# Kernel tuning notes

Measured on AMD Instinct MI355X. Metric: run time of the kernel, lower is better.

The kernel has to match this reference:

```python
import jax, jax.numpy as jnp
import numpy as np

N_NODES = 10000
N_EDGES = 100000
IN_CH = 64
EDGE_DIM = 16
HID = 128
HEADS = 4
LAYERS = 4
NUM_GRAPHS = 256


def setup_inputs() -> dict:
    key = jax.random.key(0)
    ks = jax.random.split(key, 16)
    s = 0.1
    HC = HEADS * HID
    L = LAYERS
    return {
        "x": jax.random.normal(ks[0], (N_NODES, IN_CH), jnp.float32),
        "edge_index": jax.random.randint(ks[1], (2, N_EDGES), 0, N_NODES, dtype=jnp.int32),
        "edge_attr": jax.random.normal(ks[2], (N_EDGES, EDGE_DIM), jnp.float32),
        "batch": jnp.sort(jax.random.randint(ks[3], (N_NODES,), 0, NUM_GRAPHS, dtype=jnp.int32)),
        "Win": jax.random.normal(ks[4], (IN_CH, HID), jnp.float32) * s,
        "b_in": jnp.zeros((HID,), jnp.float32),
        "Wl": jax.random.normal(ks[5], (L, HID, HC), jnp.float32) * s,
        "bl": jnp.zeros((L, HC), jnp.float32),
        "Wr": jax.random.normal(ks[6], (L, HID, HC), jnp.float32) * s,
        "br": jnp.zeros((L, HC), jnp.float32),
        "We": jax.random.normal(ks[7], (L, EDGE_DIM, HC), jnp.float32) * s,
        "att": jax.random.normal(ks[8], (L, HEADS, HID), jnp.float32) * s,
        "b_gat": jnp.zeros((L, HID), jnp.float32),
        "gamma": jnp.ones((L, HID), jnp.float32),
        "beta": jnp.zeros((L, HID), jnp.float32),
        "Wres": jax.random.normal(ks[9], (L - 1, HID, HID), jnp.float32) * s,
        "bres": jnp.zeros((L - 1, HID), jnp.float32),
        "W1": jax.random.normal(ks[10], (HID, HID), jnp.float32) * s,
        "b1": jnp.zeros((HID,), jnp.float32),
        "W2": jax.random.normal(ks[11], (HID, HID // 2), jnp.float32) * s,
        "b2": jnp.zeros((HID // 2,), jnp.float32),
        "W3": jax.random.normal(ks[12], (HID // 2, 1), jnp.float32) * s,
        "b3": jnp.zeros((1,), jnp.float32),
    }


def _layer_norm(x, g, b):
    mu = x.mean(-1, keepdims=True)
    var = ((x - mu) ** 2).mean(-1, keepdims=True)
    return g * (x - mu) / jnp.sqrt(var + 1e-5) + b


def _gatv2(h, src, dst, edge_attr, Wl, bl, Wr, br, We, att, bias):
    # GATv2Conv, concat=False, share_weights=False, negative_slope=0.2, eval mode
    N = h.shape[0]
    H, C = att.shape
    xl = (h @ Wl + bl).reshape(N, H, C)   # source-side features (lin_l)
    xr = (h @ Wr + br).reshape(N, H, C)   # target-side features (lin_r)
    e = (edge_attr @ We).reshape(-1, H, C)
    m = xl[src] + xr[dst] + e             # [E, H, C]
    m = jnp.where(m > 0, m, 0.2 * m)      # leaky_relu
    logits = jnp.einsum('ehc,hc->eh', m, att)
    lmax = jax.lax.stop_gradient(jax.ops.segment_max(logits, dst, num_segments=N))
    p = jnp.exp(logits - lmax[dst])
    denom = jax.ops.segment_sum(p, dst, num_segments=N)
    alpha = p / (denom[dst] + 1e-16)      # segment softmax over in-edges of each target
    out = jax.ops.segment_sum(alpha[:, :, None] * xl[src], dst, num_segments=N)
    return out.mean(axis=1) + bias        # concat=False -> head mean, plus bias


def reference(x, edge_index, edge_attr, batch, Win, b_in, Wl, bl, Wr, br, We, att,
              b_gat, gamma, beta, Wres, bres, W1, b1, W2, b2, W3, b3):
    src, dst = edge_index[0], edge_index[1]
    h = jax.nn.elu(x @ Win + b_in)
    for i in range(LAYERS):
        h_res = h
        h = _gatv2(h, src, dst, edge_attr, Wl[i], bl[i], Wr[i], br[i], We[i], att[i], b_gat[i])
        h = jax.nn.elu(_layer_norm(h, gamma[i], beta[i]))
        if i > 0:
            h = h + (h_res @ Wres[i - 1] + bres[i - 1])
    sums = jax.ops.segment_sum(h, batch, num_segments=NUM_GRAPHS)
    counts = jax.ops.segment_sum(jnp.ones((h.shape[0], 1), h.dtype), batch, num_segments=NUM_GRAPHS)
    hg = sums / jnp.maximum(counts, 1.0)  # global_mean_pool
    z = jax.nn.relu(hg @ W1 + b1)
    z = jax.nn.relu(z @ W2 + b2)
    return (z @ W3 + b3).reshape(-1)
```

## Files before the change

kernel.cpp:

```cpp
#include <hip/hip_runtime.h>

#define N_NODES 10000
#define N_EDGES 100000
#define IN_CH 64
#define EDGE_DIM 16
#define HID 128
#define HEADS 4
#define HC 512
#define LAYERS 4
#define NUM_GRAPHS 256
#define NCAT 1152
#define LDP 136
#define ECHUNK 32

typedef __bf16 bf16;
typedef __bf16 bf16x8 __attribute__((ext_vector_type(8)));
typedef __bf16 bf16x4 __attribute__((ext_vector_type(4)));
typedef float floatx4 __attribute__((ext_vector_type(4)));
typedef float f32x2 __attribute__((ext_vector_type(2)));

__device__ __forceinline__ float elu_f(float x) { return x > 0.f ? x : (__expf(x) - 1.f); }

__global__ __launch_bounds__(128) void k_prep_w(
    const float* __restrict__ Wl, const float* __restrict__ bl,
    const float* __restrict__ Wr, const float* __restrict__ br,
    const float* __restrict__ Wres, const float* __restrict__ bres,
    bf16* __restrict__ WT, float* __restrict__ bcat) {
    __shared__ float tile[16][129];
    int nt = blockIdx.x, i = blockIdx.y, z = blockIdx.z;
    int t = threadIdx.x;
    int n0 = nt * 128;
    const float* base = nullptr; const float* bsrc = nullptr; int ld = 0;
    if (nt < 4)       { base = Wl + (size_t)i * HID * HC + n0;            bsrc = bl + i * HC + n0;              ld = HC; }
    else if (nt < 8)  { base = Wr + (size_t)i * HID * HC + (n0 - 512);    bsrc = br + i * HC + (n0 - 512);      ld = HC; }
    else if (i > 0)   { base = Wres + (size_t)(i - 1) * HID * HID;        bsrc = bres + (size_t)(i - 1) * HID;  ld = HID; }
    if (base) {
#pragma unroll
        for (int r = 0; r < 16; r++) tile[r][t] = base[(size_t)(z * 16 + r) * ld + t];
    } else {
#pragma unroll
        for (int r = 0; r < 16; r++) tile[r][t] = 0.f;
    }
    __syncthreads();
    int n = n0 + t;
    if (z == 0) bcat[(size_t)i * NCAT + n] = base ? bsrc[t] : 0.f;
    bf16* dst = WT + ((size_t)i * NCAT + n) * HID + z * 16;
#pragma unroll
    for (int kc = 0; kc < 2; kc++) {
        bf16x8 v;
#pragma unroll
        for (int u = 0; u < 8; u++) v[u] = (bf16)tile[kc * 8 + u][t];
        *(bf16x8*)(dst + kc * 8) = v;
    }
}

__global__ __launch_bounds__(128) void k_init_h(const float* __restrict__ x,
                                                const float* __restrict__ Win,
                                                const float* __restrict__ b_in,
                                                bf16* __restrict__ h_bf) {
    __shared__ float xs[IN_CH];
    int n = blockIdx.x, t = threadIdx.x;
    if (t < IN_CH) xs[t] = x[(size_t)n * IN_CH + t];
    __syncthreads();
    float s = b_in[t];
#pragma unroll 8
    for (int k = 0; k < IN_CH; k++) s = fmaf(xs[k], Win[k * HID + t], s);
    h_bf[(size_t)n * HID + t] = (bf16)elu_f(s);
}

__global__ __launch_bounds__(256, 2) void k_gemm_mfma(
    const bf16* __restrict__ A, const bf16* __restrict__ WT,
    const float* __restrict__ bcat, bf16* __restrict__ C, int M) {
    __shared__ __align__(16) unsigned short As[128 * LDP];
    __shared__ __align__(16) unsigned short Bs[128 * LDP];
    int t = threadIdx.x;
    int r0 = blockIdx.x * 128, c0 = blockIdx.y * 128;
#pragma unroll
    for (int i = 0; i < 8; i++) {
        int idx = t + i * 256;
        int row = idx >> 4;
        int ch = idx & 15;
        int r = r0 + row; if (r >= M) r = M - 1;
        uint4 va = *(const uint4*)(A + (size_t)r * HID + ch * 8);
        *(uint4*)&As[row * LDP + ch * 8] = va;
        uint4 vb = *(const uint4*)(WT + (size_t)(c0 + row) * HID + ch * 8);
        *(uint4*)&Bs[row * LDP + ch * 8] = vb;
    }
    __syncthreads();

    int wave = t >> 6, lane = t & 63;
    int wm = wave & 1, wn = wave >> 1;
    int quad = lane >> 4, lm = lane & 15;
    floatx4 zero = {0.f, 0.f, 0.f, 0.f};
    floatx4 acc[4][4];
#pragma unroll
    for (int mi = 0; mi < 4; mi++)
#pragma unroll
        for (int ni = 0; ni < 4; ni++) acc[mi][ni] = zero;

    const unsigned short* Ab = &As[(wm * 64 + lm) * LDP + quad * 8];
    const unsigned short* Bb = &Bs[(wn * 64 + lm) * LDP + quad * 8];
#pragma unroll
    for (int ks = 0; ks < 4; ks++) {
        bf16x8 af[4], bfr[4];
#pragma unroll
        for (int mi = 0; mi < 4; mi++) af[mi] = *(const bf16x8*)(Ab + mi * 16 * LDP + ks * 32);
#pragma unroll
        for (int ni = 0; ni < 4; ni++) bfr[ni] = *(const bf16x8*)(Bb + ni * 16 * LDP + ks * 32);
#pragma unroll
        for (int mi = 0; mi < 4; mi++)
#pragma unroll
            for (int ni = 0; ni < 4; ni++)
                acc[mi][ni] = __builtin_amdgcn_mfma_f32_16x16x32_bf16(bfr[ni], af[mi], acc[mi][ni], 0, 0, 0);
    }

#pragma unroll
    for (int mi = 0; mi < 4; mi++) {
        int row = r0 + wm * 64 + mi * 16 + lm;
        if (row < M) {
            bf16* crow = C + (size_t)row * NCAT;
#pragma unroll
            for (int ni = 0; ni < 4; ni++) {
                int cb = c0 + wn * 64 + ni * 16 + quad * 4;
                float4 b4 = *(const float4*)(bcat + cb);
                floatx4 v = acc[mi][ni];
                bf16x4 o = {(bf16)(v[0] + b4.x), (bf16)(v[1] + b4.y),
                            (bf16)(v[2] + b4.z), (bf16)(v[3] + b4.w)};
                *(bf16x4*)(crow + cb) = o;
            }
        }
    }
}

__global__ void k_degree(const int* __restrict__ ei, const int* __restrict__ batch,
                         int* __restrict__ deg, int* __restrict__ cnt) {
    int e = blockIdx.x * blockDim.x + threadIdx.x;
    if (e < N_EDGES) atomicAdd(&deg[ei[N_EDGES + e]], 1);
    if (e < N_NODES) atomicAdd(&cnt[batch[e]], 1);
}

__global__ __launch_bounds__(1024) void k_scan(const int* __restrict__ deg,
                                               int* __restrict__ row_start,
                                               int* __restrict__ cursor) {
    __shared__ int wsum[16];
    __shared__ int carry_s;
    int t = threadIdx.x;
    int wave = t >> 6, lane = t & 63;
    if (t == 0) { carry_s = 0; row_start[0] = 0; }
    __syncthreads();
    for (int base = 0; base < N_NODES; base += 1024) {
        int i = base + t;
        int v = (i < N_NODES) ? deg[i] : 0;
        int incl = v;
#pragma unroll
        for (int off = 1; off < 64; off <<= 1) {
            int u = __shfl_up(incl, off, 64);
            if (lane >= off) incl += u;
        }
        if (lane == 63) wsum[wave] = incl;
        __syncthreads();
        if (wave == 0) {
            int ws = (lane < 16) ? wsum[lane] : 0;
#pragma unroll
            for (int off = 1; off < 16; off <<= 1) {
                int u = __shfl_up(ws, off, 64);
                if (lane >= off) ws += u;
            }
            if (lane < 16) wsum[lane] = ws;
        }
        __syncthreads();
        int carry = carry_s;
        int chunk_total = wsum[15];
        int total = carry + ((wave == 0) ? 0 : wsum[wave - 1]) + incl;
        if (i < N_NODES) { row_start[i + 1] = total; cursor[i] = total - v; }
        __syncthreads();
        if (t == 0) carry_s = carry + chunk_total;
    }
}

__global__ void k_scatter(const int* __restrict__ ei, const float* __restrict__ edge_attr,
                          int* __restrict__ cursor,
                          int* __restrict__ ssrc, float* __restrict__ ea_s) {
    int e = blockIdx.x * blockDim.x + threadIdx.x;
    if (e < N_EDGES) {
        int d = ei[N_EDGES + e];
        int pos = atomicAdd(&cursor[d], 1);
        ssrc[pos] = ei[e];
        const float4* s4 = (const float4*)(edge_attr + (size_t)e * EDGE_DIM);
        float4* d4 = (float4*)(ea_s + (size_t)pos * EDGE_DIM);
        d4[0] = s4[0]; d4[1] = s4[1]; d4[2] = s4[2]; d4[3] = s4[3];
    }
}

__global__ __launch_bounds__(128) void k_edge_fused(
    const bf16* __restrict__ xlr, const float* __restrict__ ea_s,
    const int* __restrict__ row_start, const int* __restrict__ ssrc,
    const float* __restrict__ We_l, const float* __restrict__ att_l,
    const float* __restrict__ bgat_l, const float* __restrict__ gamma_l,
    const float* __restrict__ beta_l,
    int has_res, float wescale,
    const int* __restrict__ batch, float* __restrict__ hsum, int do_pool,
    bf16* __restrict__ hbf_out) {
    int n = blockIdx.x;
    int t = threadIdx.x;
    int wave = t >> 6;
    int lane = t & 63;
    int c0 = wave * 256 + lane * 4;
    int head = c0 >> 7;

    f32x2 w01[16], w23[16];
#pragma unroll
    for (int k = 0; k < 16; k++) {
        float4 w = *(const float4*)(We_l + k * HC + c0);
        w01[k] = f32x2{w.x * wescale, w.y * wescale};
        w23[k] = f32x2{w.z * wescale, w.w * wescale};
    }
    float4 att4 = *(const float4*)(att_l + head * HID + (c0 & 127));
    bf16x4 vr = *(const bf16x4*)(xlr + (size_t)n * NCAT + 512 + c0);
    float xr0 = (float)vr[0], xr1 = (float)vr[1], xr2 = (float)vr[2], xr3 = (float)vr[3];

    __shared__ float4 ea_sh[ECHUNK * 4];
    __shared__ int src_sh[ECHUNK];
    __shared__ float sout[HC];
    __shared__ float red[4];

    int e0 = row_start[n], e1 = row_start[n + 1];
    float l0 = 0.f, l1 = 0.f;
    float4 a0 = {0.f, 0.f, 0.f, 0.f}, a1 = {0.f, 0.f, 0.f, 0.f};

    for (int base = e0; base < e1; base += ECHUNK) {
        int cnt = min(ECHUNK, e1 - base);
        if (t < cnt * 4) ea_sh[t] = ((const float4*)(ea_s + (size_t)base * EDGE_DIM))[t];
        if (t >= 64 && t - 64 < cnt) src_sh[t - 64] = ssrc[base + t - 64];
        __syncthreads();

        for (int jj = 0; jj < cnt; jj++) {
            float* lsum = (jj & 1) ? &l1 : &l0;
            float4* acc = (jj & 1) ? &a1 : &a0;
            int s = src_sh[jj];
            float4 q0 = ea_sh[jj * 4 + 0], q1 = ea_sh[jj * 4 + 1];
            float4 q2 = ea_sh[jj * 4 + 2], q3 = ea_sh[jj * 4 + 3];
            float eav[16] = {q0.x, q0.y, q0.z, q0.w, q1.x, q1.y, q1.z, q1.w,
                             q2.x, q2.y, q2.z, q2.w, q3.x, q3.y, q3.z, q3.w};
            bf16x4 vl = *(const bf16x4*)(xlr + (size_t)s * NCAT + c0);
            float xl0 = (float)vl[0], xl1 = (float)vl[1];
            float xl2 = (float)vl[2], xl3 = (float)vl[3];
            f32x2 e01 = {0.f, 0.f}, e23 = {0.f, 0.f};
#pragma unroll
            for (int k = 0; k < 16; k++) {
                e01 += eav[k] * w01[k];
                e23 += eav[k] * w23[k];
            }
            float m0 = xl0 + xr0 + e01.x; m0 = fmaxf(m0, 0.2f * m0);
            float m1 = xl1 + xr1 + e01.y; m1 = fmaxf(m1, 0.2f * m1);
            float m2 = xl2 + xr2 + e23.x; m2 = fmaxf(m2, 0.2f * m2);
            float m3 = xl3 + xr3 + e23.y; m3 = fmaxf(m3, 0.2f * m3);
            float partial = m0 * att4.x + m1 * att4.y + m2 * att4.z + m3 * att4.w;
#pragma unroll
            for (int off = 1; off < 32; off <<= 1) partial += __shfl_xor(partial, off, 64);
            float p = __expf(partial);
            *lsum += p;
            acc->x = fmaf(p, xl0, acc->x);
            acc->y = fmaf(p, xl1, acc->y);
            acc->z = fmaf(p, xl2, acc->z);
            acc->w = fmaf(p, xl3, acc->w);
        }
        __syncthreads();
    }

    float inv = 1.f / (l0 + l1 + 1e-16f);
    sout[c0 + 0] = (a0.x + a1.x) * inv;
    sout[c0 + 1] = (a0.y + a1.y) * inv;
    sout[c0 + 2] = (a0.z + a1.z) * inv;
    sout[c0 + 3] = (a0.w + a1.w) * inv;
    __syncthreads();

    int c = t;
    float v = 0.25f * (sout[c] + sout[c + 128] + sout[c + 256] + sout[c + 384]) + bgat_l[c];
    float s1 = v, s2 = v * v;
#pragma unroll
    for (int off = 1; off < 64; off <<= 1) {
        s1 += __shfl_xor(s1, off, 64);
        s2 += __shfl_xor(s2, off, 64);
    }
    if (lane == 0) { red[wave * 2] = s1; red[wave * 2 + 1] = s2; }
    __syncthreads();
    s1 = red[0] + red[2];
    s2 = red[1] + red[3];
    float mu = s1 * (1.f / HID);
    float var = s2 * (1.f / HID) - mu * mu;
    float rstd = rsqrtf(var + 1e-5f);
    float y = fmaf(gamma_l[c] * (v - mu), rstd, beta_l[c]);
    y = elu_f(y);
    if (has_res) y += (float)xlr[(size_t)n * NCAT + 1024 + c];
    if (do_pool) atomicAdd(&hsum[(size_t)batch[n] * HID + c], y);
    else hbf_out[(size_t)n * HID + c] = (bf16)y;
}

__global__ __launch_bounds__(128) void k_mlp(const float* __restrict__ hsum,
                                             const int* __restrict__ cnt,
                                             const float* __restrict__ W1, const float* __restrict__ b1,
                                             const float* __restrict__ W2, const float* __restrict__ b2,
                                             const float* __restrict__ W3, const float* __restrict__ b3,
                                             float* __restrict__ out) {
    int g = blockIdx.x, t = threadIdx.x;
    __shared__ float hg[HID], z1[HID], z2[64];
    float invc = 1.f / fmaxf((float)cnt[g], 1.f);
    hg[t] = hsum[(size_t)g * HID + t] * invc;
    __syncthreads();
    float s = b1[t];
#pragma unroll 8
    for (int k = 0; k < HID; k++) s = fmaf(hg[k], W1[k * HID + t], s);
    z1[t] = fmaxf(s, 0.f);
    __syncthreads();
    if (t < 64) {
        float s2 = b2[t];
#pragma unroll 8
        for (int k = 0; k < HID; k++) s2 = fmaf(z1[k], W2[k * 64 + t], s2);
        z2[t] = fmaxf(s2, 0.f);
    }
    __syncthreads();
    if (t < 64) {
        float s3 = z2[t] * W3[t];
#pragma unroll
        for (int off = 1; off < 64; off <<= 1) s3 += __shfl_xor(s3, off, 64);
        if (t == 0) out[g] = s3 + b3[0];
    }
}

extern "C" void kernel_launch(void* const* d_in, const int* in_sizes, int n_in,
                              void* d_out, int out_size, void* d_ws, size_t ws_size,
                              hipStream_t stream) {
    const float* x         = (const float*)d_in[0];
    const int*   ei        = (const int*)  d_in[1];
    const float* edge_attr = (const float*)d_in[2];
    const int*   batch     = (const int*)  d_in[3];
    const float* Win       = (const float*)d_in[4];
    const float* b_in      = (const float*)d_in[5];
    const float* Wl        = (const float*)d_in[6];
    const float* bl        = (const float*)d_in[7];
    const float* Wr        = (const float*)d_in[8];
    const float* br        = (const float*)d_in[9];
    const float* We        = (const float*)d_in[10];
    const float* att       = (const float*)d_in[11];
    const float* b_gat     = (const float*)d_in[12];
    const float* gamma     = (const float*)d_in[13];
    const float* beta      = (const float*)d_in[14];
    const float* Wres      = (const float*)d_in[15];
    const float* bres      = (const float*)d_in[16];
    const float* W1        = (const float*)d_in[17];
    const float* b1        = (const float*)d_in[18];
    const float* W2        = (const float*)d_in[19];
    const float* b2        = (const float*)d_in[20];
    const float* W3        = (const float*)d_in[21];
    const float* b3        = (const float*)d_in[22];
    float* out = (float*)d_out;

    char* ws = (char*)d_ws;
    size_t off = 0;
    auto alloc = [&](size_t bytes) -> void* {
        void* p = ws + off;
        off = (off + bytes + 255) & ~(size_t)255;
        return p;
    };
    bf16*  h_bf    = (bf16*) alloc((size_t)N_NODES * HID * 2);
    bf16*  xlr     = (bf16*) alloc((size_t)N_NODES * NCAT * 2);
    bf16*  WT      = (bf16*) alloc((size_t)LAYERS * NCAT * HID * 2);
    float* bcat    = (float*)alloc((size_t)LAYERS * NCAT * 4);
    float* ea_s    = (float*)alloc((size_t)N_EDGES * EDGE_DIM * 4);
    char*  zbase   = ws + off;
    float* hsum    = (float*)alloc((size_t)NUM_GRAPHS * HID * 4);
    int*   cnt     = (int*)  alloc((size_t)NUM_GRAPHS * 4);
    int*   deg     = (int*)  alloc((size_t)N_NODES * 4);
    size_t zlen    = (size_t)((ws + off) - zbase);
    int*   rowst   = (int*)  alloc((size_t)(N_NODES + 1) * 4);
    int*   cursor  = (int*)  alloc((size_t)N_NODES * 4);
    int*   ssrc    = (int*)  alloc((size_t)N_EDGES * 4);
    (void)ws_size;

    hipMemsetAsync(zbase, 0, zlen, stream);

    k_prep_w<<<dim3(9, LAYERS, 8), 128, 0, stream>>>(Wl, bl, Wr, br, Wres, bres, WT, bcat);
    k_degree<<<(N_EDGES + 255) / 256, 256, 0, stream>>>(ei, batch, deg, cnt);
    k_scan<<<1, 1024, 0, stream>>>(deg, rowst, cursor);
    k_scatter<<<(N_EDGES + 255) / 256, 256, 0, stream>>>(ei, edge_attr, cursor, ssrc, ea_s);
    k_init_h<<<N_NODES, 128, 0, stream>>>(x, Win, b_in, h_bf);

    const int MG = (N_NODES + 127) / 128;
    for (int i = 0; i < LAYERS; i++) {
        int ntiles = (i > 0) ? (NCAT / 128) : (1024 / 128);
        k_gemm_mfma<<<dim3(MG, ntiles), 256, 0, stream>>>(
            h_bf, WT + (size_t)i * NCAT * HID, bcat + (size_t)i * NCAT, xlr, N_NODES);
        k_edge_fused<<<N_NODES, 128, 0, stream>>>(
            xlr, ea_s, rowst, ssrc,
            We + (size_t)i * EDGE_DIM * HC, att + (size_t)i * HEADS * HID,
            b_gat + (size_t)i * HID, gamma + (size_t)i * HID, beta + (size_t)i * HID,
            (i > 0) ? 1 : 0, 1.0f,
            batch, hsum, (i == LAYERS - 1) ? 1 : 0, h_bf);
    }

    k_mlp<<<NUM_GRAPHS, 128, 0, stream>>>(hsum, cnt, W1, b1, W2, b2, W3, b3, out);
}
```

Measured before the change: 459.9 us.

## Load edge data directly from global memory, drop LDS staging, and vectorize scan

The edge kernel no longer stages edge attributes and source indices through shared memory with per-chunk barriers. Each thread now reads them straight from global memory, where the loads are broadcast or cached. The f32x2 packed edge projection becomes scalar FMAs, and an empty asm pins the weights in registers. The scan kernel now handles four elements per thread, cutting its loop iterations. The tradeoff is that every lane issues redundant global loads for the same edge data, with possible latency exposure in exchange for removing the synchronisation.

```diff
diff --git a/kernel.cpp b/kernel.cpp
--- a/kernel.cpp
+++ b/kernel.cpp
@@ -11,13 +11,11 @@
 #define NUM_GRAPHS 256
 #define NCAT 1152
 #define LDP 136
-#define ECHUNK 32
 
 typedef __bf16 bf16;
 typedef __bf16 bf16x8 __attribute__((ext_vector_type(8)));
 typedef __bf16 bf16x4 __attribute__((ext_vector_type(4)));
 typedef float floatx4 __attribute__((ext_vector_type(4)));
-typedef float f32x2 __attribute__((ext_vector_type(2)));
 
 __device__ __forceinline__ float elu_f(float x) { return x > 0.f ? x : (__expf(x) - 1.f); }
 
@@ -148,10 +146,13 @@
     int wave = t >> 6, lane = t & 63;
     if (t == 0) { carry_s = 0; row_start[0] = 0; }
     __syncthreads();
-    for (int base = 0; base < N_NODES; base += 1024) {
-        int i = base + t;
-        int v = (i < N_NODES) ? deg[i] : 0;
-        int incl = v;
+    for (int base = 0; base < N_NODES; base += 4096) {
+        int i0 = base + t * 4;
+        int v[4];
+#pragma unroll
+        for (int u = 0; u < 4; u++) v[u] = (i0 + u < N_NODES) ? deg[i0 + u] : 0;
+        int tsum = v[0] + v[1] + v[2] + v[3];
+        int incl = tsum;
 #pragma unroll
         for (int off = 1; off < 64; off <<= 1) {
             int u = __shfl_up(incl, off, 64);
@@ -171,8 +172,12 @@
         __syncthreads();
         int carry = carry_s;
         int chunk_total = wsum[15];
-        int total = carry + ((wave == 0) ? 0 : wsum[wave - 1]) + incl;
-        if (i < N_NODES) { row_start[i + 1] = total; cursor[i] = total - v; }
+        int p = carry + ((wave == 0) ? 0 : wsum[wave - 1]) + incl - tsum;
+#pragma unroll
+        for (int u = 0; u < 4; u++) {
+            int i = i0 + u;
+            if (i < N_NODES) { cursor[i] = p; p += v[u]; row_start[i + 1] = p; }
+        }
         __syncthreads();
         if (t == 0) carry_s = carry + chunk_total;
     }
@@ -198,7 +203,7 @@
     const float* __restrict__ We_l, const float* __restrict__ att_l,
     const float* __restrict__ bgat_l, const float* __restrict__ gamma_l,
     const float* __restrict__ beta_l,
-    int has_res, float wescale,
+    int has_res,
     const int* __restrict__ batch, float* __restrict__ hsum, int do_pool,
     bf16* __restrict__ hbf_out) {
     int n = blockIdx.x;
@@ -208,67 +213,63 @@
     int c0 = wave * 256 + lane * 4;
     int head = c0 >> 7;
 
-    f32x2 w01[16], w23[16];
+    float wx[16], wy[16], wz[16], ww[16];
 #pragma unroll
     for (int k = 0; k < 16; k++) {
         float4 w = *(const float4*)(We_l + k * HC + c0);
-        w01[k] = f32x2{w.x * wescale, w.y * wescale};
-        w23[k] = f32x2{w.z * wescale, w.w * wescale};
-    }
+        wx[k] = w.x; wy[k] = w.y; wz[k] = w.z; ww[k] = w.w;
+    }
+#pragma unroll
+    for (int k = 0; k < 16; k++) {
+        asm volatile("" : "+v"(wx[k]), "+v"(wy[k]), "+v"(wz[k]), "+v"(ww[k]));
+    }
+
     float4 att4 = *(const float4*)(att_l + head * HID + (c0 & 127));
     bf16x4 vr = *(const bf16x4*)(xlr + (size_t)n * NCAT + 512 + c0);
     float xr0 = (float)vr[0], xr1 = (float)vr[1], xr2 = (float)vr[2], xr3 = (float)vr[3];
 
-    __shared__ float4 ea_sh[ECHUNK * 4];
-    __shared__ int src_sh[ECHUNK];
-    __shared__ float sout[HC];
-    __shared__ float red[4];
-
     int e0 = row_start[n], e1 = row_start[n + 1];
     float l0 = 0.f, l1 = 0.f;
     float4 a0 = {0.f, 0.f, 0.f, 0.f}, a1 = {0.f, 0.f, 0.f, 0.f};
 
-    for (int base = e0; base < e1; base += ECHUNK) {
-        int cnt = min(ECHUNK, e1 - base);
-        if (t < cnt * 4) ea_sh[t] = ((const float4*)(ea_s + (size_t)base * EDGE_DIM))[t];
-        if (t >= 64 && t - 64 < cnt) src_sh[t - 64] = ssrc[base + t - 64];
-        __syncthreads();
-
-        for (int jj = 0; jj < cnt; jj++) {
-            float* lsum = (jj & 1) ? &l1 : &l0;
-            float4* acc = (jj & 1) ? &a1 : &a0;
-            int s = src_sh[jj];
-            float4 q0 = ea_sh[jj * 4 + 0], q1 = ea_sh[jj * 4 + 1];
-            float4 q2 = ea_sh[jj * 4 + 2], q3 = ea_sh[jj * 4 + 3];
-            float eav[16] = {q0.x, q0.y, q0.z, q0.w, q1.x, q1.y, q1.z, q1.w,
-                             q2.x, q2.y, q2.z, q2.w, q3.x, q3.y, q3.z, q3.w};
-            bf16x4 vl = *(const bf16x4*)(xlr + (size_t)s * NCAT + c0);
-            float xl0 = (float)vl[0], xl1 = (float)vl[1];
-            float xl2 = (float)vl[2], xl3 = (float)vl[3];
-            f32x2 e01 = {0.f, 0.f}, e23 = {0.f, 0.f};
-#pragma unroll
-            for (int k = 0; k < 16; k++) {
-                e01 += eav[k] * w01[k];
-                e23 += eav[k] * w23[k];
-            }
-            float m0 = xl0 + xr0 + e01.x; m0 = fmaxf(m0, 0.2f * m0);
-            float m1 = xl1 + xr1 + e01.y; m1 = fmaxf(m1, 0.2f * m1);
-            float m2 = xl2 + xr2 + e23.x; m2 = fmaxf(m2, 0.2f * m2);
-            float m3 = xl3 + xr3 + e23.y; m3 = fmaxf(m3, 0.2f * m3);
-            float partial = m0 * att4.x + m1 * att4.y + m2 * att4.z + m3 * att4.w;
-#pragma unroll
-            for (int off = 1; off < 32; off <<= 1) partial += __shfl_xor(partial, off, 64);
-            float p = __expf(partial);
-            *lsum += p;
-            acc->x = fmaf(p, xl0, acc->x);
-            acc->y = fmaf(p, xl1, acc->y);
-            acc->z = fmaf(p, xl2, acc->z);
-            acc->w = fmaf(p, xl3, acc->w);
+    for (int j = e0; j < e1; j++) {
+        float* lsum = ((j - e0) & 1) ? &l1 : &l0;
+        float4* acc = ((j - e0) & 1) ? &a1 : &a0;
+        int s = ssrc[j];
+        const float4* eap = (const float4*)(ea_s + (size_t)j * EDGE_DIM);
+        float4 q0 = eap[0], q1 = eap[1], q2 = eap[2], q3 = eap[3];
+        float eav[16] = {q0.x, q0.y, q0.z, q0.w, q1.x, q1.y, q1.z, q1.w,
+                         q2.x, q2.y, q2.z, q2.w, q3.x, q3.y, q3.z, q3.w};
+        bf16x4 vl = *(const bf16x4*)(xlr + (size_t)s * NCAT + c0);
+        float xl0 = (float)vl[0], xl1 = (float)vl[1];
+        float xl2 = (float)vl[2], xl3 = (float)vl[3];
+        float e0x = 0.f, e1x = 0.f, e2x = 0.f, e3x = 0.f;
+#pragma unroll
+        for (int k = 0; k < 16; k++) {
+            e0x = fmaf(eav[k], wx[k], e0x);
+            e1x = fmaf(eav[k], wy[k], e1x);
+            e2x = fmaf(eav[k], wz[k], e2x);
+            e3x = fmaf(eav[k], ww[k], e3x);
         }
-        __syncthreads();
+        float m0 = xl0 + xr0 + e0x; m0 = fmaxf(m0, 0.2f * m0);
+        float m1 = xl1 + xr1 + e1x; m1 = fmaxf(m1, 0.2f * m1);
+        float m2 = xl2 + xr2 + e2x; m2 = fmaxf(m2, 0.2f * m2);
+        float m3 = xl3 + xr3 + e3x; m3 = fmaxf(m3, 0.2f * m3);
+        float partial = m0 * att4.x + m1 * att4.y + m2 * att4.z + m3 * att4.w;
+#pragma unroll
+        for (int off = 1; off < 32; off <<= 1) partial += __shfl_xor(partial, off, 64);
+        float p = __expf(partial);
+        *lsum += p;
+        acc->x = fmaf(p, xl0, acc->x);
+        acc->y = fmaf(p, xl1, acc->y);
+        acc->z = fmaf(p, xl2, acc->z);
+        acc->w = fmaf(p, xl3, acc->w);
     }
 
     float inv = 1.f / (l0 + l1 + 1e-16f);
+
+    __shared__ float sout[HC];
+    __shared__ float red[4];
     sout[c0 + 0] = (a0.x + a1.x) * inv;
     sout[c0 + 1] = (a0.y + a1.y) * inv;
     sout[c0 + 2] = (a0.z + a1.z) * inv;
@@ -395,7 +396,7 @@
             xlr, ea_s, rowst, ssrc,
             We + (size_t)i * EDGE_DIM * HC, att + (size_t)i * HEADS * HID,
             b_gat + (size_t)i * HID, gamma + (size_t)i * HID, beta + (size_t)i * HID,
-            (i > 0) ? 1 : 0, 1.0f,
+            (i > 0) ? 1 : 0,
             batch, hsum, (i == LAYERS - 1) ? 1 : 0, h_bf);
     }
 
```

After: 470.3 us. 2.3% more time.
